# Kernel optimization log

Measured on AMD Instinct MI355X. Metric: run time of the kernel, lower is better.

## Reference

```python
import jax, jax.numpy as jnp
import numpy as np

B, S, T = 4096, 32, 32   # batch (flattened words), source chars, target chars
V = 256                  # char vocab (source and target)
E, H, A = 128, 64, 64    # source embed, GRU units, attention dim
BOW = 1                  # begin-of-word token id


def setup_inputs() -> dict:
    key = jax.random.key(0)
    ks = iter(jax.random.split(key, 32))
    p = lambda shape: jax.random.normal(next(ks), shape, dtype=jnp.float32) * 0.05
    return {
        "src_ids": jax.random.randint(next(ks), (B, S), 0, V, dtype=jnp.int64),
        "tgt_ids": jax.random.randint(next(ks), (B, T), 0, V, dtype=jnp.int64),
        "src_emb": p((V, E)),
        "enc_Wf": p((E, 3 * H)), "enc_Uf": p((H, 3 * H)), "enc_bf": p((2, 3 * H)),
        "enc_Wb": p((E, 3 * H)), "enc_Ub": p((H, 3 * H)), "enc_bb": p((2, 3 * H)),
        "attn_We": p((H, A)), "attn_be": p((A,)),
        "attn_Wd": p((H, A)), "attn_bd": p((A,)),
        "attn_v": p((A, 1)), "attn_bv": p((1,)),
        "dec_W": p((H + H, 3 * H)), "dec_U": p((H, 3 * H)), "dec_b": p((2, 3 * H)),
        "out_W": p((H, V)), "out_b": p((V,)),
    }


def _gru_cell(h, x, W, U, b):
    # TF GRUCell with reset_after=True (default): separate input/recurrent biases
    xp = x @ W + b[0]
    hp = h @ U + b[1]
    xz, xr, xh = jnp.split(xp, 3, axis=-1)
    hz, hr, hh = jnp.split(hp, 3, axis=-1)
    z = jax.nn.sigmoid(xz + hz)
    r = jax.nn.sigmoid(xr + hr)
    n = jnp.tanh(xh + r * hh)
    return z * h + (1.0 - z) * n


def _gru_scan(xs, h0, W, U, b):
    # xs: [S, B, D] -> outputs [S, B, H]
    def step(h, x):
        h_new = _gru_cell(h, x, W, U, b)
        return h_new, h_new
    _, ys = jax.lax.scan(step, h0, xs)
    return ys


def reference(src_ids, tgt_ids, src_emb,
              enc_Wf, enc_Uf, enc_bf, enc_Wb, enc_Ub, enc_bb,
              attn_We, attn_be, attn_Wd, attn_bd, attn_v, attn_bv,
              dec_W, dec_U, dec_b, out_W, out_b):
    batch = src_ids.shape[0]
    # --- encoder: embedding + bidirectional GRU (merge_mode='sum') ---
    emb = src_emb[src_ids]                       # [B,S,E]
    xs = jnp.swapaxes(emb, 0, 1)                 # [S,B,E]
    h0 = jnp.zeros((batch, H), emb.dtype)
    fwd = _gru_scan(xs, h0, enc_Wf, enc_Uf, enc_bf)
    bwd = _gru_scan(xs[::-1], h0, enc_Wb, enc_Ub, enc_bb)[::-1]
    encoded = jnp.swapaxes(fwd + bwd, 0, 1)      # [B,S,H]

    # --- attention memory setup ---
    enc_proj = encoded @ attn_We + attn_be       # [B,S,A]

    # --- decoder inputs: BOW-prefixed teacher-forced targets, tied embedding ---
    dec_in = jnp.concatenate(
        [jnp.full((batch, 1), BOW, dtype=tgt_ids.dtype), tgt_ids[:, :-1]], axis=1)
    tied_table = out_W.T * jnp.sqrt(jnp.asarray(H, encoded.dtype))  # [V,H]
    dec_emb = tied_table[dec_in]                 # [B,T,H]

    # --- decoder: Bahdanau-attention GRU, scan over time ---
    def step(h, x):
        dproj = h @ attn_Wd + attn_bd                        # [B,A]
        s = jnp.tanh(dproj[:, None, :] + enc_proj)           # [B,S,A]
        logit = (s @ attn_v)[..., 0] + attn_bv[0]            # [B,S]
        w = jax.nn.softmax(logit, axis=1)                    # softmax over S
        ctx = jnp.einsum('bs,bsh->bh', w, encoded)           # [B,H]
        att_in = jnp.concatenate([x, ctx], axis=1)           # [B,2H]
        h_new = _gru_cell(h, att_in, dec_W, dec_U, dec_b)
        return h_new, h_new

    _, hs = jax.lax.scan(step, encoded[:, 0], jnp.swapaxes(dec_emb, 0, 1))
    hidden = jnp.swapaxes(hs, 0, 1)              # [B,T,H]
    logits = hidden @ out_W + out_b              # [B,T,V]
    return logits
```

## Files before the change

kernel.cpp:

```cpp
#include <hip/hip_runtime.h>
#include <hip/hip_bf16.h>

typedef unsigned short u16;
typedef __bf16  bf16x8 __attribute__((ext_vector_type(8)));
typedef float   f32x4  __attribute__((ext_vector_type(4)));
typedef unsigned int   u32x4 __attribute__((ext_vector_type(4)));
typedef unsigned short u16x4 __attribute__((ext_vector_type(4)));

union FragU { bf16x8 v; u16 u[8]; u32x4 q; };

__device__ __forceinline__ float b2f(u16 u) {
    unsigned int x = ((unsigned int)u) << 16;
    return __builtin_bit_cast(float, x);
}
__device__ __forceinline__ u16 f2b(float f) {
    unsigned int x = __builtin_bit_cast(unsigned int, f);
    unsigned int r = (x + 0x7fffu + ((x >> 16) & 1u)) >> 16;
    return (u16)r;
}
__device__ __forceinline__ float rcp_(float x) { return __builtin_amdgcn_rcpf(x); }
__device__ __forceinline__ float sigm_(float x) { return rcp_(1.0f + __expf(-x)); }
__device__ __forceinline__ float tanh_(float x) {
    float e = __expf(2.0f * x);
    return 1.0f - 2.0f * rcp_(e + 1.0f);
}
__device__ __forceinline__ bf16x8 load_afrag(const u16* s) {
    FragU f; f.q = *(const u32x4*)s; return f.v;
}
__device__ __forceinline__ f32x4 mfma16(bf16x8 a, bf16x8 b, f32x4 c) {
    return __builtin_amdgcn_mfma_f32_16x16x32_bf16(a, b, c, 0, 0, 0);
}
__device__ __forceinline__ void split2(float f, u16& hi, u16& lo) {
    hi = f2b(f); lo = f2b(f - b2f(hi));
}

template<int MODE, int K, int N>
__global__ __launch_bounds__(256, (MODE >= 2) ? 2 : 1) void gemm_hl(
    const float* __restrict__ srcf, const u16* __restrict__ sh,
    const u16* __restrict__ sl, const float* __restrict__ W,
    const float* __restrict__ bias, float* __restrict__ outf,
    u16* __restrict__ outh)
{
    constexpr int KP = K + 8;
    constexpr int LK = (K == 128) ? 7 : 6;
    __shared__ __attribute__((aligned(16))) u16 Ash[64 * KP];
    __shared__ __attribute__((aligned(16))) u16 Asl[64 * KP];

    const int tid  = threadIdx.x;
    const int lane = tid & 63, w = tid >> 6;
    const int q = lane >> 4, ln = lane & 15;
    const int rbase = blockIdx.x * 64;

    for (int i = tid; i < 64 * K; i += 256) {
        int r = i >> LK, c = i & (K - 1);
        int rg = rbase + r;
        float f;
        if constexpr (MODE == 0)      f = srcf[rg * K + c];
        else if constexpr (MODE == 1) f = srcf[c * 256 + rg] * 8.0f;
        else                          f = b2f(sh[rg * 64 + c]) + b2f(sl[rg * 64 + c]);
        u16 hi, lo; split2(f, hi, lo);
        Ash[r * KP + c] = hi; Asl[r * KP + c] = lo;
    }

    constexpr int NT  = N / 64;
    constexpr int NKF = K / 32;
    FragU bfh[NT][NKF], bfl[NT][NKF];
    float bv[NT];
    const int cw = w * (N >> 2);
#pragma unroll
    for (int tl = 0; tl < NT; ++tl) {
        int col = cw + tl * 16 + ln;
#pragma unroll
        for (int kf = 0; kf < NKF; ++kf)
#pragma unroll
            for (int j = 0; j < 8; ++j) {
                float f = W[(kf * 32 + q * 8 + j) * N + col];
                split2(f, bfh[tl][kf].u[j], bfl[tl][kf].u[j]);
            }
        bv[tl] = bias[col];
    }
    __syncthreads();

#pragma unroll
    for (int r = 0; r < 4; ++r) {
        bf16x8 afh[NKF], afl[NKF];
#pragma unroll
        for (int kf = 0; kf < NKF; ++kf) {
            afh[kf] = load_afrag(&Ash[(r * 16 + ln) * KP + kf * 32 + q * 8]);
            afl[kf] = load_afrag(&Asl[(r * 16 + ln) * KP + kf * 32 + q * 8]);
        }
#pragma unroll
        for (int tl = 0; tl < NT; ++tl) {
            f32x4 acc = {0.f, 0.f, 0.f, 0.f};
#pragma unroll
            for (int kf = 0; kf < NKF; ++kf) {
                acc = mfma16(afl[kf], bfh[tl][kf].v, acc);
                acc = mfma16(afh[kf], bfl[tl][kf].v, acc);
                acc = mfma16(afh[kf], bfh[tl][kf].v, acc);
            }
            const int col = cw + tl * 16 + ln;
#pragma unroll
            for (int i = 0; i < 4; ++i) {
                int rowg = rbase + r * 16 + q * 4 + i;
                float val = acc[i] + bv[tl];
                if constexpr (MODE == 2) {
                    int b = rowg >> 5, s2 = rowg & 31;
                    outh[(b * 64 + col) * 32 + s2] = f2b(val * 2.0f);
                } else if constexpr (MODE == 3) {
                    outf[rowg * N + col] = val;
                } else {
                    outf[rowg * 192 + col] = val;
                }
            }
        }
    }
}

template<int DIR>
__global__ __launch_bounds__(256, 1) void enc_kernel(
    const int* __restrict__ src_ids, const float* __restrict__ xpv,
    const float* __restrict__ U, const float* __restrict__ b_,
    u16* __restrict__ oh, u16* __restrict__ ol,
    const u16* __restrict__ fh, const u16* __restrict__ fl)
{
    __shared__ __attribute__((aligned(16))) u16 hsh[16 * 72];
    __shared__ __attribute__((aligned(16))) u16 hsl[16 * 72];
    const int tid  = threadIdx.x;
    const int lane = tid & 63, w = tid >> 6;
    const int q = lane >> 4, ln = lane & 15;
    const int b0 = blockIdx.x * 16;
    const int jw = w * 16;

    for (int i = tid; i < 16 * 64; i += 256) {
        int r = i >> 6, c = i & 63;
        hsh[r * 72 + c] = 0; hsl[r * 72 + c] = 0;
    }
    FragU ufh[3][2], ufl[3][2];
    float b1[3];
#pragma unroll
    for (int g = 0; g < 3; ++g) {
        int col = g * 64 + jw + ln;
#pragma unroll
        for (int kf = 0; kf < 2; ++kf)
#pragma unroll
            for (int j = 0; j < 8; ++j) {
                float f = U[(kf * 32 + q * 8 + j) * 192 + col];
                split2(f, ufh[g][kf].u[j], ufl[g][kf].u[j]);
            }
        b1[g] = b_[192 + col];
    }
    float hp[4] = {0, 0, 0, 0};

    float xg[3][4];
    {
        const int s0 = DIR ? 31 : 0;
#pragma unroll
        for (int i = 0; i < 4; ++i) {
            int id = src_ids[(b0 + q * 4 + i) * 32 + s0];
#pragma unroll
            for (int g = 0; g < 3; ++g) xg[g][i] = xpv[id * 192 + g * 64 + jw + ln];
        }
    }
    __syncthreads();

    for (int step = 0; step < 32; ++step) {
        const int s = DIR ? (31 - step) : step;
        float xgn[3][4];
        {
            int sn = DIR ? (step >= 31 ? 0 : 30 - step) : (step >= 31 ? 31 : step + 1);
#pragma unroll
            for (int i = 0; i < 4; ++i) {
                int id = src_ids[(b0 + q * 4 + i) * 32 + sn];
#pragma unroll
                for (int g = 0; g < 3; ++g) xgn[g][i] = xpv[id * 192 + g * 64 + jw + ln];
            }
        }
        bf16x8 a0h = load_afrag(&hsh[ln * 72 + q * 8]);
        bf16x8 a1h = load_afrag(&hsh[ln * 72 + 32 + q * 8]);
        bf16x8 a0l = load_afrag(&hsl[ln * 72 + q * 8]);
        bf16x8 a1l = load_afrag(&hsl[ln * 72 + 32 + q * 8]);
        f32x4 acc[3];
#pragma unroll
        for (int g = 0; g < 3; ++g) {
            f32x4 a = {0.f, 0.f, 0.f, 0.f};
            a = mfma16(a0l, ufh[g][0].v, a);
            a = mfma16(a0h, ufl[g][0].v, a);
            a = mfma16(a0h, ufh[g][0].v, a);
            a = mfma16(a1l, ufh[g][1].v, a);
            a = mfma16(a1h, ufl[g][1].v, a);
            a = mfma16(a1h, ufh[g][1].v, a);
            acc[g] = a;
        }
        float nh[4];
#pragma unroll
        for (int i = 0; i < 4; ++i) {
            const int rowg = b0 + q * 4 + i;
            float zz = sigm_(xg[0][i] + acc[0][i] + b1[0]);
            float rr = sigm_(xg[1][i] + acc[1][i] + b1[1]);
            float nn = tanh_(xg[2][i] + rr * (acc[2][i] + b1[2]));
            nh[i] = zz * hp[i] + (1.0f - zz) * nn;  hp[i] = nh[i];
            const int gidx = (rowg * 32 + s) * 64 + jw + ln;
            float ov = nh[i];
            if constexpr (DIR == 1) ov += b2f(fh[gidx]) + b2f(fl[gidx]);
            u16 hi, lo; split2(ov, hi, lo);
            oh[gidx] = hi; ol[gidx] = lo;
        }
        __syncthreads();
#pragma unroll
        for (int i = 0; i < 4; ++i) {
            u16 hi, lo; split2(nh[i], hi, lo);
            hsh[(q * 4 + i) * 72 + jw + ln] = hi;
            hsl[(q * 4 + i) * 72 + jw + ln] = lo;
        }
        __syncthreads();
#pragma unroll
        for (int g = 0; g < 3; ++g)
#pragma unroll
            for (int i = 0; i < 4; ++i) xg[g][i] = xgn[g][i];
    }
}

__global__ __launch_bounds__(256, 1) void dec_kernel(
    const int* __restrict__ tgt_ids, const float* __restrict__ xpvd,
    const u16* __restrict__ enc_hi, const u16* __restrict__ enc_lo,
    const u16* __restrict__ encpT,
    const float* __restrict__ dec_U, const float* __restrict__ dec_W,
    const float* __restrict__ dec_b,
    const float* __restrict__ Wd, const float* __restrict__ bd,
    const float* __restrict__ v_, const float* __restrict__ bv_,
    u16* __restrict__ hid_hi, u16* __restrict__ hid_lo)
{
    __shared__ __attribute__((aligned(16))) float enc_lds[16 * 2048];
    __shared__ __attribute__((aligned(16))) u16 hqh[16 * 72];
    __shared__ __attribute__((aligned(16))) u16 hql[16 * 72];
    __shared__ __attribute__((aligned(16))) u16 cxh[16 * 72];
    __shared__ __attribute__((aligned(16))) u16 cxl[16 * 72];
    __shared__ float dpl[16 * 72];
    __shared__ float wl[16 * 36];
    __shared__ float vl[64];
    const int tid  = threadIdx.x;
    const int lane = tid & 63, w = tid >> 6;
    const int q = lane >> 4, ln = lane & 15;
    const int b0 = blockIdx.x * 16;
    const int jw = w * 16;

    {
        const u16* gh = enc_hi + (size_t)b0 * 2048;
        const u16* gl = enc_lo + (size_t)b0 * 2048;
        for (int i = tid; i < 16 * 2048 / 4; i += 256) {
            u16x4 vh = *(const u16x4*)(gh + i * 4);
            u16x4 vo = *(const u16x4*)(gl + i * 4);
            f32x4 f;
            f[0] = b2f(vh[0]) + b2f(vo[0]);
            f[1] = b2f(vh[1]) + b2f(vo[1]);
            f[2] = b2f(vh[2]) + b2f(vo[2]);
            f[3] = b2f(vh[3]) + b2f(vo[3]);
            *(f32x4*)(&enc_lds[i * 4]) = f;
        }
    }
    if (tid < 64) vl[tid] = v_[tid];
    const float bv0 = bv_[0];

    FragU wdh[2], wdl[2], ufh[3][2], ufl[3][2], wch[3][2], wcl[3][2];
    float b1[3];
#pragma unroll
    for (int kf = 0; kf < 2; ++kf)
#pragma unroll
        for (int j = 0; j < 8; ++j) {
            float f = Wd[(kf * 32 + q * 8 + j) * 64 + jw + ln];
            split2(f, wdh[kf].u[j], wdl[kf].u[j]);
        }
#pragma unroll
    for (int g = 0; g < 3; ++g) {
        int col = g * 64 + jw + ln;
#pragma unroll
        for (int kf = 0; kf < 2; ++kf)
#pragma unroll
            for (int j = 0; j < 8; ++j) {
                int k = kf * 32 + q * 8 + j;
                float fu = dec_U[k * 192 + col];
                split2(fu, ufh[g][kf].u[j], ufl[g][kf].u[j]);
                float fc = dec_W[(64 + k) * 192 + col];
                split2(fc, wch[g][kf].u[j], wcl[g][kf].u[j]);
            }
        b1[g] = dec_b[192 + col];
    }
    const float bd_ = bd[jw + ln];

    FragU epr[2][8];
    {
        const int bb = tid >> 5, ss = tid & 31;
        const u16* ep0 = &encpT[(size_t)(b0 + bb) * 2048 + ss];
        const u16* ep1 = &encpT[(size_t)(b0 + 8 + bb) * 2048 + ss];
#pragma unroll
        for (int a8 = 0; a8 < 8; ++a8)
#pragma unroll
            for (int j = 0; j < 8; ++j) {
                epr[0][a8].u[j] = ep0[(a8 * 8 + j) * 32];
                epr[1][a8].u[j] = ep1[(a8 * 8 + j) * 32];
            }
    }

    float xg[3][4];
#pragma unroll
    for (int g = 0; g < 3; ++g) {
        float f = xpvd[1 * 192 + g * 64 + jw + ln];
#pragma unroll
        for (int i = 0; i < 4; ++i) xg[g][i] = f;
    }
    __syncthreads();

    float SVB = bv0;
#pragma unroll
    for (int a = 0; a < 64; ++a) SVB += vl[a];

    for (int i = tid; i < 16 * 64; i += 256) {
        int r = i >> 6, c = i & 63;
        u16 hi, lo; split2(enc_lds[r * 2048 + c], hi, lo);
        hqh[r * 72 + c] = hi; hql[r * 72 + c] = lo;
    }
    float hp[4];
#pragma unroll
    for (int i = 0; i < 4; ++i) hp[i] = enc_lds[(q * 4 + i) * 2048 + jw + ln];
    __syncthreads();

    for (int t = 0; t < 32; ++t) {
        float xgn[3][4];
        {
            int tn = (t >= 31) ? 30 : t;
#pragma unroll
            for (int i = 0; i < 4; ++i) {
                int id = tgt_ids[(b0 + q * 4 + i) * 32 + tn];
#pragma unroll
                for (int g = 0; g < 3; ++g) xgn[g][i] = xpvd[id * 192 + g * 64 + jw + ln];
            }
        }
        bf16x8 ah0 = load_afrag(&hqh[ln * 72 + q * 8]);
        bf16x8 ah1 = load_afrag(&hqh[ln * 72 + 32 + q * 8]);
        bf16x8 al0 = load_afrag(&hql[ln * 72 + q * 8]);
        bf16x8 al1 = load_afrag(&hql[ln * 72 + 32 + q * 8]);
        {
            f32x4 a = {0.f, 0.f, 0.f, 0.f};
            a = mfma16(al0, wdh[0].v, a);
            a = mfma16(ah0, wdl[0].v, a);
            a = mfma16(ah0, wdh[0].v, a);
            a = mfma16(al1, wdh[1].v, a);
            a = mfma16(ah1, wdl[1].v, a);
            a = mfma16(ah1, wdh[1].v, a);
#pragma unroll
            for (int i = 0; i < 4; ++i)
                dpl[(q * 4 + i) * 72 + jw + ln] = (a[i] + bd_) * 2.0f;
        }
        __syncthreads();
#pragma unroll
        for (int pp = 0; pp < 2; ++pp) {
            const int bb = (tid >> 5) + pp * 8;
            const int sidx = tid & 31;
            const float* dp = &dpl[bb * 72];
            float av0 = 0.f, av1 = 0.f, av2 = 0.f, av3 = 0.f;
#pragma unroll
            for (int a8 = 0; a8 < 8; ++a8) {
#pragma unroll
                for (int j = 0; j < 8; ++j) {
                    const int a = a8 * 8 + j;
                    float u = dp[a] + b2f(epr[pp][a8].u[j]);
                    float e = __expf(u);
                    float rc = vl[a] * rcp_(e + 1.0f);
                    if ((j & 3) == 0)      av0 += rc;
                    else if ((j & 3) == 1) av1 += rc;
                    else if ((j & 3) == 2) av2 += rc;
                    else                   av3 += rc;
                }
            }
            float logit = SVB - 2.0f * ((av0 + av1) + (av2 + av3));
            float m = logit;
#pragma unroll
            for (int off = 16; off > 0; off >>= 1) m = fmaxf(m, __shfl_xor(m, off, 32));
            float e2 = __expf(logit - m);
            float ssum = e2;
#pragma unroll
            for (int off = 16; off > 0; off >>= 1) ssum += __shfl_xor(ssum, off, 32);
            wl[bb * 36 + sidx] = e2 * rcp_(ssum);
        }
        __syncthreads();
#pragma unroll
        for (int rr2 = 0; rr2 < 4; ++rr2) {
            const int b = rr2 * 4 + w;
            float c0 = 0.f, c1 = 0.f, c2 = 0.f, c3 = 0.f;
#pragma unroll
            for (int s4 = 0; s4 < 8; ++s4) {
                const int s = s4 * 4 + q;
                const float ww = wl[b * 36 + s];
                f32x4 ev = *(const f32x4*)(&enc_lds[b * 2048 + s * 64 + ln * 4]);
                c0 += ww * ev[0]; c1 += ww * ev[1];
                c2 += ww * ev[2]; c3 += ww * ev[3];
            }
            c0 += __shfl_xor(c0, 16); c0 += __shfl_xor(c0, 32);
            c1 += __shfl_xor(c1, 16); c1 += __shfl_xor(c1, 32);
            c2 += __shfl_xor(c2, 16); c2 += __shfl_xor(c2, 32);
            c3 += __shfl_xor(c3, 16); c3 += __shfl_xor(c3, 32);
            if (q == 0) {
                u16x4 vh, vo;
                u16 th, tl2;
                split2(c0, th, tl2); vh[0] = th; vo[0] = tl2;
                split2(c1, th, tl2); vh[1] = th; vo[1] = tl2;
                split2(c2, th, tl2); vh[2] = th; vo[2] = tl2;
                split2(c3, th, tl2); vh[3] = th; vo[3] = tl2;
                *(u16x4*)(&cxh[b * 72 + ln * 4]) = vh;
                *(u16x4*)(&cxl[b * 72 + ln * 4]) = vo;
            }
        }
        __syncthreads();
        bf16x8 ac0 = load_afrag(&cxh[ln * 72 + q * 8]);
        bf16x8 ac1 = load_afrag(&cxh[ln * 72 + 32 + q * 8]);
        bf16x8 al2 = load_afrag(&cxl[ln * 72 + q * 8]);
        bf16x8 al3 = load_afrag(&cxl[ln * 72 + 32 + q * 8]);
        f32x4 ax[3], ahh[3];
#pragma unroll
        for (int g = 0; g < 3; ++g) {
            f32x4 a = {0.f, 0.f, 0.f, 0.f};
            a = mfma16(al2, wch[g][0].v, a);
            a = mfma16(ac0, wcl[g][0].v, a);
            a = mfma16(ac0, wch[g][0].v, a);
            a = mfma16(al3, wch[g][1].v, a);
            a = mfma16(ac1, wcl[g][1].v, a);
            a = mfma16(ac1, wch[g][1].v, a);
            ax[g] = a;
            f32x4 h = {0.f, 0.f, 0.f, 0.f};
            h = mfma16(al0, ufh[g][0].v, h);
            h = mfma16(ah0, ufl[g][0].v, h);
            h = mfma16(ah0, ufh[g][0].v, h);
            h = mfma16(al1, ufh[g][1].v, h);
            h = mfma16(ah1, ufl[g][1].v, h);
            h = mfma16(ah1, ufh[g][1].v, h);
            ahh[g] = h;
        }
        float nh[4];
#pragma unroll
        for (int i = 0; i < 4; ++i) {
            int rowg = b0 + q * 4 + i;
            float zz = sigm_(xg[0][i] + ax[0][i] + ahh[0][i] + b1[0]);
            float rr = sigm_(xg[1][i] + ax[1][i] + ahh[1][i] + b1[1]);
            float nn = tanh_(xg[2][i] + ax[2][i] + rr * (ahh[2][i] + b1[2]));
            nh[i] = zz * hp[i] + (1.0f - zz) * nn;  hp[i] = nh[i];
            int gidx = (rowg * 32 + t) * 64 + jw + ln;
            u16 hi, lo; split2(nh[i], hi, lo);
            hid_hi[gidx] = hi; hid_lo[gidx] = lo;
        }
        __syncthreads();
#pragma unroll
        for (int i = 0; i < 4; ++i) {
            u16 hi, lo; split2(nh[i], hi, lo);
            hqh[(q * 4 + i) * 72 + jw + ln] = hi;
            hql[(q * 4 + i) * 72 + jw + ln] = lo;
        }
        __syncthreads();
#pragma unroll
        for (int g = 0; g < 3; ++g)
#pragma unroll
            for (int i = 0; i < 4; ++i) xg[g][i] = xgn[g][i];
    }
}

extern "C" void kernel_launch(void* const* d_in, const int* in_sizes, int n_in,
                              void* d_out, int out_size, void* d_ws, size_t ws_size,
                              hipStream_t stream) {
    const int*   src_ids = (const int*)d_in[0];
    const int*   tgt_ids = (const int*)d_in[1];
    const float* src_emb = (const float*)d_in[2];
    const float* enc_Wf  = (const float*)d_in[3];
    const float* enc_Uf  = (const float*)d_in[4];
    const float* enc_bf  = (const float*)d_in[5];
    const float* enc_Wb  = (const float*)d_in[6];
    const float* enc_Ub  = (const float*)d_in[7];
    const float* enc_bb  = (const float*)d_in[8];
    const float* attn_We = (const float*)d_in[9];
    const float* attn_be = (const float*)d_in[10];
    const float* attn_Wd = (const float*)d_in[11];
    const float* attn_bd = (const float*)d_in[12];
    const float* attn_v  = (const float*)d_in[13];
    const float* attn_bv = (const float*)d_in[14];
    const float* dec_W   = (const float*)d_in[15];
    const float* dec_U   = (const float*)d_in[16];
    const float* dec_b   = (const float*)d_in[17];
    const float* out_W   = (const float*)d_in[18];
    const float* out_b   = (const float*)d_in[19];

    u16* ws = (u16*)d_ws;
    u16* fwd_hi = ws;
    u16* fwd_lo = ws +  8388608;
    u16* enc_hi = ws + 16777216;
    u16* enc_lo = ws + 25165824;
    u16* encpT  = ws + 33554432;
    float* xpv  = (float*)(ws + 41943040);
    u16* hid_hi = fwd_hi;
    u16* hid_lo = fwd_lo;

    dim3 blk(256);
    gemm_hl<0, 128, 192><<<4, blk, 0, stream>>>(
        src_emb, nullptr, nullptr, enc_Wf, enc_bf, xpv, nullptr);
    enc_kernel<0><<<256, blk, 0, stream>>>(src_ids, xpv, enc_Uf, enc_bf,
                                           fwd_hi, fwd_lo, nullptr, nullptr);
    gemm_hl<0, 128, 192><<<4, blk, 0, stream>>>(
        src_emb, nullptr, nullptr, enc_Wb, enc_bb, xpv, nullptr);
    enc_kernel<1><<<256, blk, 0, stream>>>(src_ids, xpv, enc_Ub, enc_bb,
                                           enc_hi, enc_lo, fwd_hi, fwd_lo);
    gemm_hl<2, 64, 64><<<2048, blk, 0, stream>>>(
        nullptr, enc_hi, enc_lo, attn_We, attn_be, nullptr, encpT);
    gemm_hl<1, 64, 192><<<4, blk, 0, stream>>>(
        out_W, nullptr, nullptr, dec_W, dec_b, xpv, nullptr);
    dec_kernel<<<256, blk, 0, stream>>>(tgt_ids, xpv, enc_hi, enc_lo, encpT,
                                        dec_U, dec_W, dec_b, attn_Wd, attn_bd,
                                        attn_v, attn_bv, hid_hi, hid_lo);
    gemm_hl<3, 64, 256><<<2048, blk, 0, stream>>>(
        nullptr, hid_hi, hid_lo, out_W, out_b, (float*)d_out, nullptr);
}
```

Baseline: 594.9 us.

## Run both encoder directions concurrently with 8-row blocks; factor attention exp

Merges the forward and backward encoder passes into one kernel of 1024 blocks, each handling 8 batch rows in one direction. The forward/backward sum moves into the consumers (attention projection GEMM and decoder LDS load). The decoder also drops to 8 rows per block, doubling the grid with two blocks per CU. Its tanh in the attention score is rewritten as exp(dproj)*exp(encproj), so the encoder-side exp is precomputed once instead of recomputed every step. Half the MFMA rows in each block are now padding, trading wasted compute for more concurrent blocks on the serial recurrences.

```diff
diff --git a/kernel.cpp b/kernel.cpp
--- a/kernel.cpp
+++ b/kernel.cpp
@@ -37,7 +37,8 @@
 template<int MODE, int K, int N>
 __global__ __launch_bounds__(256, (MODE >= 2) ? 2 : 1) void gemm_hl(
     const float* __restrict__ srcf, const u16* __restrict__ sh,
-    const u16* __restrict__ sl, const float* __restrict__ W,
+    const u16* __restrict__ sl, const u16* __restrict__ sh2,
+    const u16* __restrict__ sl2, const float* __restrict__ W,
     const float* __restrict__ bias, float* __restrict__ outf,
     u16* __restrict__ outh)
 {
@@ -57,6 +58,9 @@
         float f;
         if constexpr (MODE == 0)      f = srcf[rg * K + c];
         else if constexpr (MODE == 1) f = srcf[c * 256 + rg] * 8.0f;
+        else if constexpr (MODE == 2)
+            f = b2f(sh[rg * 64 + c]) + b2f(sl[rg * 64 + c])
+              + b2f(sh2[rg * 64 + c]) + b2f(sl2[rg * 64 + c]);
         else                          f = b2f(sh[rg * 64 + c]) + b2f(sl[rg * 64 + c]);
         u16 hi, lo; split2(f, hi, lo);
         Ash[r * KP + c] = hi; Asl[r * KP + c] = lo;
@@ -116,20 +120,28 @@
     }
 }
 
-template<int DIR>
-__global__ __launch_bounds__(256, 1) void enc_kernel(
-    const int* __restrict__ src_ids, const float* __restrict__ xpv,
-    const float* __restrict__ U, const float* __restrict__ b_,
-    u16* __restrict__ oh, u16* __restrict__ ol,
-    const u16* __restrict__ fh, const u16* __restrict__ fl)
+__global__ __launch_bounds__(256, 2) void enc8(
+    const int* __restrict__ src_ids, const float* __restrict__ xf,
+    const float* __restrict__ xb,
+    const float* __restrict__ Uf_, const float* __restrict__ bf_,
+    const float* __restrict__ Ub_, const float* __restrict__ bb_,
+    u16* __restrict__ fh, u16* __restrict__ fl,
+    u16* __restrict__ bh, u16* __restrict__ bl)
 {
     __shared__ __attribute__((aligned(16))) u16 hsh[16 * 72];
     __shared__ __attribute__((aligned(16))) u16 hsl[16 * 72];
     const int tid  = threadIdx.x;
     const int lane = tid & 63, w = tid >> 6;
     const int q = lane >> 4, ln = lane & 15;
-    const int b0 = blockIdx.x * 16;
+    const int dir = (int)(blockIdx.x >> 9);
+    const int b0  = (int)(blockIdx.x & 511) * 8;
+    const float* xpv = dir ? xb  : xf;
+    const float* U   = dir ? Ub_ : Uf_;
+    const float* b_  = dir ? bb_ : bf_;
+    u16* oh = dir ? bh : fh;
+    u16* ol = dir ? bl : fl;
     const int jw = w * 16;
+    const bool rowok = (q < 2);
 
     for (int i = tid; i < 16 * 64; i += 256) {
         int r = i >> 6, c = i & 63;
@@ -153,10 +165,11 @@
 
     float xg[3][4];
     {
-        const int s0 = DIR ? 31 : 0;
+        const int s0 = dir ? 31 : 0;
 #pragma unroll
         for (int i = 0; i < 4; ++i) {
-            int id = src_ids[(b0 + q * 4 + i) * 32 + s0];
+            int rowv = b0 + ((q * 4 + i) & 7);
+            int id = src_ids[rowv * 32 + s0];
 #pragma unroll
             for (int g = 0; g < 3; ++g) xg[g][i] = xpv[id * 192 + g * 64 + jw + ln];
         }
@@ -164,13 +177,14 @@
     __syncthreads();
 
     for (int step = 0; step < 32; ++step) {
-        const int s = DIR ? (31 - step) : step;
+        const int s = dir ? (31 - step) : step;
         float xgn[3][4];
         {
-            int sn = DIR ? (step >= 31 ? 0 : 30 - step) : (step >= 31 ? 31 : step + 1);
+            int sn = dir ? (step >= 31 ? 0 : 30 - step) : (step >= 31 ? 31 : step + 1);
 #pragma unroll
             for (int i = 0; i < 4; ++i) {
-                int id = src_ids[(b0 + q * 4 + i) * 32 + sn];
+                int rowv = b0 + ((q * 4 + i) & 7);
+                int id = src_ids[rowv * 32 + sn];
 #pragma unroll
                 for (int g = 0; g < 3; ++g) xgn[g][i] = xpv[id * 192 + g * 64 + jw + ln];
             }
@@ -199,18 +213,20 @@
             float rr = sigm_(xg[1][i] + acc[1][i] + b1[1]);
             float nn = tanh_(xg[2][i] + rr * (acc[2][i] + b1[2]));
             nh[i] = zz * hp[i] + (1.0f - zz) * nn;  hp[i] = nh[i];
-            const int gidx = (rowg * 32 + s) * 64 + jw + ln;
-            float ov = nh[i];
-            if constexpr (DIR == 1) ov += b2f(fh[gidx]) + b2f(fl[gidx]);
-            u16 hi, lo; split2(ov, hi, lo);
-            oh[gidx] = hi; ol[gidx] = lo;
+            if (rowok) {
+                const int gidx = (rowg * 32 + s) * 64 + jw + ln;
+                u16 hi, lo; split2(nh[i], hi, lo);
+                oh[gidx] = hi; ol[gidx] = lo;
+            }
         }
         __syncthreads();
-#pragma unroll
-        for (int i = 0; i < 4; ++i) {
-            u16 hi, lo; split2(nh[i], hi, lo);
-            hsh[(q * 4 + i) * 72 + jw + ln] = hi;
-            hsl[(q * 4 + i) * 72 + jw + ln] = lo;
+        if (rowok) {
+#pragma unroll
+            for (int i = 0; i < 4; ++i) {
+                u16 hi, lo; split2(nh[i], hi, lo);
+                hsh[(q * 4 + i) * 72 + jw + ln] = hi;
+                hsl[(q * 4 + i) * 72 + jw + ln] = lo;
+            }
         }
         __syncthreads();
 #pragma unroll
@@ -220,9 +236,10 @@
     }
 }
 
-__global__ __launch_bounds__(256, 1) void dec_kernel(
+__global__ __launch_bounds__(256, 2) void dec_kernel(
     const int* __restrict__ tgt_ids, const float* __restrict__ xpvd,
-    const u16* __restrict__ enc_hi, const u16* __restrict__ enc_lo,
+    const u16* __restrict__ fh, const u16* __restrict__ fl,
+    const u16* __restrict__ bh, const u16* __restrict__ bl,
     const u16* __restrict__ encpT,
     const float* __restrict__ dec_U, const float* __restrict__ dec_W,
     const float* __restrict__ dec_b,
@@ -230,31 +247,35 @@
     const float* __restrict__ v_, const float* __restrict__ bv_,
     u16* __restrict__ hid_hi, u16* __restrict__ hid_lo)
 {
-    __shared__ __attribute__((aligned(16))) float enc_lds[16 * 2048];
+    __shared__ __attribute__((aligned(16))) float enc_lds[8 * 2048];
     __shared__ __attribute__((aligned(16))) u16 hqh[16 * 72];
     __shared__ __attribute__((aligned(16))) u16 hql[16 * 72];
     __shared__ __attribute__((aligned(16))) u16 cxh[16 * 72];
     __shared__ __attribute__((aligned(16))) u16 cxl[16 * 72];
-    __shared__ float dpl[16 * 72];
-    __shared__ float wl[16 * 36];
+    __shared__ __attribute__((aligned(16))) float edl[8 * 72];
+    __shared__ float wl[8 * 36];
     __shared__ float vl[64];
     const int tid  = threadIdx.x;
     const int lane = tid & 63, w = tid >> 6;
     const int q = lane >> 4, ln = lane & 15;
-    const int b0 = blockIdx.x * 16;
+    const int b0 = blockIdx.x * 8;
     const int jw = w * 16;
+    const bool rowok = (q < 2);
 
     {
-        const u16* gh = enc_hi + (size_t)b0 * 2048;
-        const u16* gl = enc_lo + (size_t)b0 * 2048;
-        for (int i = tid; i < 16 * 2048 / 4; i += 256) {
-            u16x4 vh = *(const u16x4*)(gh + i * 4);
-            u16x4 vo = *(const u16x4*)(gl + i * 4);
+        const u16* g0 = fh + (size_t)b0 * 2048;
+        const u16* g1 = fl + (size_t)b0 * 2048;
+        const u16* g2 = bh + (size_t)b0 * 2048;
+        const u16* g3 = bl + (size_t)b0 * 2048;
+        for (int i = tid; i < 8 * 2048 / 4; i += 256) {
+            u16x4 v0 = *(const u16x4*)(g0 + i * 4);
+            u16x4 v1 = *(const u16x4*)(g1 + i * 4);
+            u16x4 v2 = *(const u16x4*)(g2 + i * 4);
+            u16x4 v3 = *(const u16x4*)(g3 + i * 4);
             f32x4 f;
-            f[0] = b2f(vh[0]) + b2f(vo[0]);
-            f[1] = b2f(vh[1]) + b2f(vo[1]);
-            f[2] = b2f(vh[2]) + b2f(vo[2]);
-            f[3] = b2f(vh[3]) + b2f(vo[3]);
+#pragma unroll
+            for (int k = 0; k < 4; ++k)
+                f[k] = (b2f(v0[k]) + b2f(v1[k])) + (b2f(v2[k]) + b2f(v3[k]));
             *(f32x4*)(&enc_lds[i * 4]) = f;
         }
     }
@@ -287,18 +308,12 @@
     }
     const float bd_ = bd[jw + ln];
 
-    FragU epr[2][8];
+    float Ee[64];
     {
-        const int bb = tid >> 5, ss = tid & 31;
-        const u16* ep0 = &encpT[(size_t)(b0 + bb) * 2048 + ss];
-        const u16* ep1 = &encpT[(size_t)(b0 + 8 + bb) * 2048 + ss];
-#pragma unroll
-        for (int a8 = 0; a8 < 8; ++a8)
-#pragma unroll
-            for (int j = 0; j < 8; ++j) {
-                epr[0][a8].u[j] = ep0[(a8 * 8 + j) * 32];
-                epr[1][a8].u[j] = ep1[(a8 * 8 + j) * 32];
-            }
+        const int bb2 = tid >> 5, ss = tid & 31;
+        const u16* ep = &encpT[(size_t)(b0 + bb2) * 2048 + ss];
+#pragma unroll
+        for (int a = 0; a < 64; ++a) Ee[a] = __expf(b2f(ep[a * 32]));
     }
 
     float xg[3][4];
@@ -316,12 +331,18 @@
 
     for (int i = tid; i < 16 * 64; i += 256) {
         int r = i >> 6, c = i & 63;
-        u16 hi, lo; split2(enc_lds[r * 2048 + c], hi, lo);
-        hqh[r * 72 + c] = hi; hql[r * 72 + c] = lo;
+        if (r < 8) {
+            u16 hi, lo; split2(enc_lds[r * 2048 + c], hi, lo);
+            hqh[r * 72 + c] = hi; hql[r * 72 + c] = lo;
+        } else {
+            hqh[r * 72 + c] = 0; hql[r * 72 + c] = 0;
+            cxh[r * 72 + c] = 0; cxl[r * 72 + c] = 0;
+        }
     }
     float hp[4];
 #pragma unroll
-    for (int i = 0; i < 4; ++i) hp[i] = enc_lds[(q * 4 + i) * 2048 + jw + ln];
+    for (int i = 0; i < 4; ++i)
+        hp[i] = rowok ? enc_lds[(q * 4 + i) * 2048 + jw + ln] : 0.f;
     __syncthreads();
 
     for (int t = 0; t < 32; ++t) {
@@ -330,7 +351,8 @@
             int tn = (t >= 31) ? 30 : t;
 #pragma unroll
             for (int i = 0; i < 4; ++i) {
-                int id = tgt_ids[(b0 + q * 4 + i) * 32 + tn];
+                int rowv = b0 + ((q * 4 + i) & 7);
+                int id = tgt_ids[rowv * 32 + tn];
 #pragma unroll
                 for (int g = 0; g < 3; ++g) xgn[g][i] = xpvd[id * 192 + g * 64 + jw + ln];
             }
@@ -347,30 +369,24 @@
             a = mfma16(al1, wdh[1].v, a);
             a = mfma16(ah1, wdl[1].v, a);
             a = mfma16(ah1, wdh[1].v, a);
-#pragma unroll
-            for (int i = 0; i < 4; ++i)
-                dpl[(q * 4 + i) * 72 + jw + ln] = (a[i] + bd_) * 2.0f;
+            if (rowok) {
+#pragma unroll
+                for (int i = 0; i < 4; ++i)
+                    edl[(q * 4 + i) * 72 + jw + ln] = __expf((a[i] + bd_) * 2.0f);
+            }
         }
         __syncthreads();
-#pragma unroll
-        for (int pp = 0; pp < 2; ++pp) {
-            const int bb = (tid >> 5) + pp * 8;
-            const int sidx = tid & 31;
-            const float* dp = &dpl[bb * 72];
+        {
+            const int bb2 = tid >> 5, sidx = tid & 31;
+            const float* dp = &edl[bb2 * 72];
             float av0 = 0.f, av1 = 0.f, av2 = 0.f, av3 = 0.f;
 #pragma unroll
-            for (int a8 = 0; a8 < 8; ++a8) {
-#pragma unroll
-                for (int j = 0; j < 8; ++j) {
-                    const int a = a8 * 8 + j;
-                    float u = dp[a] + b2f(epr[pp][a8].u[j]);
-                    float e = __expf(u);
-                    float rc = vl[a] * rcp_(e + 1.0f);
-                    if ((j & 3) == 0)      av0 += rc;
-                    else if ((j & 3) == 1) av1 += rc;
-                    else if ((j & 3) == 2) av2 += rc;
-                    else                   av3 += rc;
-                }
+            for (int a4 = 0; a4 < 16; ++a4) {
+                f32x4 dv = *(const f32x4*)(dp + a4 * 4);
+                av0 += vl[a4 * 4 + 0] * rcp_(__builtin_fmaf(dv[0], Ee[a4 * 4 + 0], 1.0f));
+                av1 += vl[a4 * 4 + 1] * rcp_(__builtin_fmaf(dv[1], Ee[a4 * 4 + 1], 1.0f));
+                av2 += vl[a4 * 4 + 2] * rcp_(__builtin_fmaf(dv[2], Ee[a4 * 4 + 2], 1.0f));
+                av3 += vl[a4 * 4 + 3] * rcp_(__builtin_fmaf(dv[3], Ee[a4 * 4 + 3], 1.0f));
             }
             float logit = SVB - 2.0f * ((av0 + av1) + (av2 + av3));
             float m = logit;
@@ -380,11 +396,11 @@
             float ssum = e2;
 #pragma unroll
             for (int off = 16; off > 0; off >>= 1) ssum += __shfl_xor(ssum, off, 32);
-            wl[bb * 36 + sidx] = e2 * rcp_(ssum);
+            wl[bb2 * 36 + sidx] = e2 * rcp_(ssum);
         }
         __syncthreads();
 #pragma unroll
-        for (int rr2 = 0; rr2 < 4; ++rr2) {
+        for (int rr2 = 0; rr2 < 2; ++rr2) {
             const int b = rr2 * 4 + w;
             float c0 = 0.f, c1 = 0.f, c2 = 0.f, c3 = 0.f;
 #pragma unroll
@@ -443,16 +459,13 @@
             float rr = sigm_(xg[1][i] + ax[1][i] + ahh[1][i] + b1[1]);
             float nn = tanh_(xg[2][i] + ax[2][i] + rr * (ahh[2][i] + b1[2]));
             nh[i] = zz * hp[i] + (1.0f - zz) * nn;  hp[i] = nh[i];
-            int gidx = (rowg * 32 + t) * 64 + jw + ln;
-            u16 hi, lo; split2(nh[i], hi, lo);
-            hid_hi[gidx] = hi; hid_lo[gidx] = lo;
-        }
-        __syncthreads();
-#pragma unroll
-        for (int i = 0; i < 4; ++i) {
-            u16 hi, lo; split2(nh[i], hi, lo);
-            hqh[(q * 4 + i) * 72 + jw + ln] = hi;
-            hql[(q * 4 + i) * 72 + jw + ln] = lo;
+            if (rowok) {
+                int gidx = (rowg * 32 + t) * 64 + jw + ln;
+                u16 hi, lo; split2(nh[i], hi, lo);
+                hid_hi[gidx] = hi; hid_lo[gidx] = lo;
+                hqh[(q * 4 + i) * 72 + jw + ln] = hi;
+                hql[(q * 4 + i) * 72 + jw + ln] = lo;
+            }
         }
         __syncthreads();
 #pragma unroll
@@ -489,29 +502,30 @@
     u16* ws = (u16*)d_ws;
     u16* fwd_hi = ws;
     u16* fwd_lo = ws +  8388608;
-    u16* enc_hi = ws + 16777216;
-    u16* enc_lo = ws + 25165824;
+    u16* bwd_hi = ws + 16777216;
+    u16* bwd_lo = ws + 25165824;
     u16* encpT  = ws + 33554432;
-    float* xpv  = (float*)(ws + 41943040);
+    float* xpv_f = (float*)(ws + 41943040);
+    float* xpv_b = (float*)(ws + 42041344);
+    float* xpvd  = (float*)(ws + 42139648);
     u16* hid_hi = fwd_hi;
     u16* hid_lo = fwd_lo;
 
     dim3 blk(256);
     gemm_hl<0, 128, 192><<<4, blk, 0, stream>>>(
-        src_emb, nullptr, nullptr, enc_Wf, enc_bf, xpv, nullptr);
-    enc_kernel<0><<<256, blk, 0, stream>>>(src_ids, xpv, enc_Uf, enc_bf,
-                                           fwd_hi, fwd_lo, nullptr, nullptr);
+        src_emb, nullptr, nullptr, nullptr, nullptr, enc_Wf, enc_bf, xpv_f, nullptr);
     gemm_hl<0, 128, 192><<<4, blk, 0, stream>>>(
-        src_emb, nullptr, nullptr, enc_Wb, enc_bb, xpv, nullptr);
-    enc_kernel<1><<<256, blk, 0, stream>>>(src_ids, xpv, enc_Ub, enc_bb,
-                                           enc_hi, enc_lo, fwd_hi, fwd_lo);
+        src_emb, nullptr, nullptr, nullptr, nullptr, enc_Wb, enc_bb, xpv_b, nullptr);
+    gemm_hl<1, 64, 192><<<4, blk, 0, stream>>>(
+        out_W, nullptr, nullptr, nullptr, nullptr, dec_W, dec_b, xpvd, nullptr);
+    enc8<<<1024, blk, 0, stream>>>(src_ids, xpv_f, xpv_b, enc_Uf, enc_bf,
+                                   enc_Ub, enc_bb, fwd_hi, fwd_lo, bwd_hi, bwd_lo);
     gemm_hl<2, 64, 64><<<2048, blk, 0, stream>>>(
-        nullptr, enc_hi, enc_lo, attn_We, attn_be, nullptr, encpT);
-    gemm_hl<1, 64, 192><<<4, blk, 0, stream>>>(
-        out_W, nullptr, nullptr, dec_W, dec_b, xpv, nullptr);
-    dec_kernel<<<256, blk, 0, stream>>>(tgt_ids, xpv, enc_hi, enc_lo, encpT,
-                                        dec_U, dec_W, dec_b, attn_Wd, attn_bd,
-                                        attn_v, attn_bv, hid_hi, hid_lo);
+        nullptr, fwd_hi, fwd_lo, bwd_hi, bwd_lo, attn_We, attn_be, nullptr, encpT);
+    dec_kernel<<<512, blk, 0, stream>>>(tgt_ids, xpvd, fwd_hi, fwd_lo, bwd_hi,
+                                        bwd_lo, encpT, dec_U, dec_W, dec_b,
+                                        attn_Wd, attn_bd, attn_v, attn_bv,
+                                        hid_hi, hid_lo);
     gemm_hl<3, 64, 256><<<2048, blk, 0, stream>>>(
-        nullptr, hid_hi, hid_lo, out_W, out_b, (float*)d_out, nullptr);
-}
+        nullptr, hid_hi, hid_lo, nullptr, nullptr, out_W, out_b, (float*)d_out, nullptr);
+}
```

Result: slower. 947.5 us (+59.3%).
